# Optimization experiments

Measured on AMD Instinct MI355X. Metric: run time of the kernel, lower is better.

## Reference

```python
import jax, jax.numpy as jnp
import numpy as np

INF = 1e8        # effectively-infinite squared distance (max real value ~3*192^2)
SIGMA = 10.0     # module init arg
CHUNK = 512      # lines processed per block in the min-plus pass
P_FG = 0.005     # sparse foreground probability for the binary mask
N = 192


def _dt1d_last(f):
    """Exact 1D squared-EDT min-plus transform along the last axis.

    d[..., i] = min_j f[..., j] + (i - j)^2, computed brute-force per line,
    chunked over lines to bound memory ([CHUNK, n, n] per block).
    """
    n = f.shape[-1]
    idx = jnp.arange(n, dtype=f.dtype)
    q = (idx[:, None] - idx[None, :]) ** 2              # [n_out, n_in]
    flat = f.reshape(-1, n)
    m = flat.shape[0]
    pad = (-m) % CHUNK
    blocks = jnp.pad(flat, ((0, pad), (0, 0)), constant_values=0.0)
    blocks = blocks.reshape(-1, CHUNK, n)               # [nblk, CHUNK, n]

    def body(b):                                        # b: [CHUNK, n]
        return jnp.min(b[:, None, :] + q[None, :, :], axis=-1)

    out = jax.lax.map(body, blocks).reshape(-1, n)[:m]
    return out.reshape(f.shape)


def _edt(seed, shape_ndim):
    """Euclidean distance to nearest True voxel of `seed` (scipy edt semantics:
    distance_transform_edt(a) == distance to nearest zero of a, i.e. seed = (a == 0))."""
    f = jnp.where(seed, 0.0, INF).astype(jnp.float32)
    for ax in range(shape_ndim):
        f = jnp.moveaxis(_dt1d_last(jnp.moveaxis(f, ax, -1)), -1, ax)
    return jnp.sqrt(f)


def setup_inputs() -> dict:
    key = jax.random.key(0)
    # sparse binary foreground mask (float 0/1), matching a label mask input
    x = (jax.random.uniform(key, (N, N, N)) < P_FG).astype(jnp.float32)
    return {"x": x}


def reference(x) -> jnp.ndarray:
    nd = x.ndim
    d_fg = _edt(x == 0, nd)   # edt(x):      distance to nearest zero of x
    d_bg = _edt(x != 0, nd)   # edt(x == 0): distance to nearest nonzero of x
    return jnp.tanh((d_fg - d_bg) / SIGMA)
```

## Files before the change

kernel.cpp:

```cpp
#include <hip/hip_runtime.h>


typedef unsigned short u16;
typedef unsigned int   u32;
typedef unsigned long long u64;
typedef u16 u16x2 __attribute__((ext_vector_type(2)));

#define NN    192
#define NN2   (192 * 192)
#define NN3   (192 * 192 * 192)

#define PAIRS 8
#define PADL  40
#define SROW  278
#define SENT16 50000
#define SENTPK 0xC350C350u

__device__ __forceinline__ u16x2 pkmin(u16x2 a, u16x2 b) { return __builtin_elementwise_min(a, b); }
__device__ __forceinline__ u16x2 pkmax(u16x2 a, u16x2 b) { return __builtin_elementwise_max(a, b); }
__device__ __forceinline__ u32 pkm32(u32 a, u32 b) {
    return __builtin_bit_cast(u32, pkmin(__builtin_bit_cast(u16x2, a), __builtin_bit_cast(u16x2, b)));
}

__device__ __forceinline__ u64 shr_pair(u64 lo, u64 hi, int s) {
    return (lo >> s) | (s ? (hi << ((64 - s) & 63)) : 0ULL);
}
__device__ __forceinline__ int dist3(u64 a0, u64 a1, u64 a2, int s) {
    u64 w0 = shr_pair(a0, a1, s);
    u64 w1 = shr_pair(a1, a2, s);
    u64 w2 = a2 >> s;
    int t0 = w0 ? __builtin_ctzll(w0) : 255;
    int t1 = w1 ? 64 + __builtin_ctzll(w1) : 255;
    int t2 = w2 ? 128 + __builtin_ctzll(w2) : 255;
    int r = t0 < t1 ? t0 : t1;
    return r < t2 ? r : t2;
}
__device__ __forceinline__ void line_edt(u64 m0, u64 m1, u64 m2, int lane,
                                         u16& o0, u16& o1, u16& o2) {
    u64 r0 = __builtin_bitreverse64(m2);
    u64 r1 = __builtin_bitreverse64(m1);
    u64 r2 = __builtin_bitreverse64(m0);
    const int s = lane, t = 63 - lane;
    int f0 = dist3(m0, m1, m2, s);
    int f1 = dist3(m1, m2, 0ULL, s);
    int f2 = dist3(m2, 0ULL, 0ULL, s);
    int b0 = dist3(r2, 0ULL, 0ULL, t);
    int b1 = dist3(r1, r2, 0ULL, t);
    int b2 = dist3(r0, r1, r2, t);
    int d0 = f0 < b0 ? f0 : b0;
    int d1 = f1 < b1 ? f1 : b1;
    int d2 = f2 < b2 ? f2 : b2;
    o0 = (d0 > 191) ? (u16)65535 : (u16)(d0 * d0);
    o1 = (d1 > 191) ? (u16)65535 : (u16)(d1 * d1);
    o2 = (d2 > 191) ? (u16)65535 : (u16)(d2 * d2);
}

__global__ __launch_bounds__(256) void sdt_scan_k(const float* __restrict__ x,
                                                  u16* __restrict__ A,
                                                  u16* __restrict__ B) {
    const int lane = threadIdx.x & 63;
    const int wid = blockIdx.x * 4 + (threadIdx.x >> 6);
    const size_t base = (size_t)wid * NN;
    float v0 = x[base + lane];
    float v1 = x[base + lane + 64];
    float v2 = x[base + lane + 128];
    u64 m0 = __ballot(v0 != 0.0f);
    u64 m1 = __ballot(v1 != 0.0f);
    u64 m2 = __ballot(v2 != 0.0f);
    u16 a0, a1, a2, b0, b1, b2;
    line_edt(~m0, ~m1, ~m2, lane, a0, a1, a2);
    line_edt(m0, m1, m2, lane, b0, b1, b2);
    A[base + lane] = a0; A[base + lane + 64] = a1; A[base + lane + 128] = a2;
    B[base + lane] = b0; B[base + lane + 64] = b1; B[base + lane + 128] = b2;
}

__device__ __forceinline__ void pad_init(u32* ldsw) {
    for (int idx = threadIdx.x; idx < PAIRS * 86; idx += 512) {
        int p = idx / 86, c = idx - p * 86;
        int word = (c < PADL) ? c : (c + NN);
        ldsw[p * SROW + word] = SENTPK;
    }
}

template<long ES>
__device__ __forceinline__ void stage_in(const u16* __restrict__ f, size_t base, u32* ldsw) {
    for (int idx = threadIdx.x; idx < NN * 2; idx += 512) {
        int j = idx >> 1, q = idx & 1;
        uint4 v = *(const uint4*)(f + base + (size_t)j * ES + 8 * q);
        int a = PADL + j;
        ldsw[(4 * q + 0) * SROW + a] = pkm32(v.x, SENTPK);
        ldsw[(4 * q + 1) * SROW + a] = pkm32(v.y, SENTPK);
        ldsw[(4 * q + 2) * SROW + a] = pkm32(v.z, SENTPK);
        ldsw[(4 * q + 3) * SROW + a] = pkm32(v.w, SENTPK);
    }
}

template<long ES>
__device__ __forceinline__ void stage_out(u16* __restrict__ f, size_t base, const u32* ldsw) {
    for (int idx = threadIdx.x; idx < NN * 2; idx += 512) {
        int j = idx >> 1, q = idx & 1;
        int a = PADL + j;
        uint4 v;
        v.x = ldsw[(4 * q + 0) * SROW + a];
        v.y = ldsw[(4 * q + 1) * SROW + a];
        v.z = ldsw[(4 * q + 2) * SROW + a];
        v.w = ldsw[(4 * q + 3) * SROW + a];
        *(uint4*)(f + base + (size_t)j * ES + 8 * q) = v;
    }
}

__device__ __forceinline__ void full_row(const u16x2* rp, int i0, int i1, int i2,
                                         u16x2& d0, u16x2& d1, u16x2& d2) {
    const float fi0 = (float)i0, fi1 = (float)i1, fi2 = (float)i2;
    float e0l = 3e38f, e0h = 3e38f, e1l = 3e38f, e1h = 3e38f, e2l = 3e38f, e2h = 3e38f;
    for (int j = 0; j < NN; ++j) {
        u16x2 gv = rp[j];
        float gl = (float)gv.x, gh = (float)gv.y;
        float jf = (float)j;
        float t0 = jf - fi0, t1 = jf - fi1, t2 = jf - fi2;
        float s0 = t0 * t0, s1 = t1 * t1, s2 = t2 * t2;
        e0l = fminf(e0l, s0 + gl); e0h = fminf(e0h, s0 + gh);
        e1l = fminf(e1l, s1 + gl); e1h = fminf(e1h, s1 + gh);
        e2l = fminf(e2l, s2 + gl); e2h = fminf(e2h, s2 + gh);
    }
    d0.x = (u16)fminf((float)d0.x, e0l); d0.y = (u16)fminf((float)d0.y, e0h);
    d1.x = (u16)fminf((float)d1.x, e1l); d1.y = (u16)fminf((float)d1.y, e1h);
    d2.x = (u16)fminf((float)d2.x, e2l); d2.y = (u16)fminf((float)d2.y, e2h);
}

__device__ __forceinline__ void expand_tile(u32* ldsw) {
    const int lane = threadIdx.x & 63;
    const int w = threadIdx.x >> 6;
    const int i0 = lane, i1 = lane + 64, i2 = lane + 128;
    u16x2* rp = (u16x2*)(ldsw + w * SROW + PADL);
    u16x2 d0 = rp[i0], d1 = rp[i1], d2 = rp[i2];

    int r = 1;
    bool conv = false;
    while (true) {
#pragma unroll
        for (int m = 0; m < 8; ++m) {
            const int rad = r + m;
            const u16 c = (u16)(rad * rad);
            const u16x2 q = {c, c};
            d0 = pkmin(d0, rp[i0 - rad] + q); d0 = pkmin(d0, rp[i0 + rad] + q);
            d1 = pkmin(d1, rp[i1 - rad] + q); d1 = pkmin(d1, rp[i1 + rad] + q);
            d2 = pkmin(d2, rp[i2 - rad] + q); d2 = pkmin(d2, rp[i2 + rad] + q);
        }
        u16x2 mv = pkmax(pkmax(d0, d1), d2);
        unsigned mm = (mv.x > mv.y) ? mv.x : mv.y;
        unsigned thr = (unsigned)((r + 8) * (r + 8));
        if (__all(mm <= thr)) { conv = true; break; }
        r += 8;
        if (r > 33) break;
    }
    if (!conv) {
        u16x2 mv = pkmax(pkmax(d0, d1), d2);
        unsigned mm = (mv.x > mv.y) ? mv.x : mv.y;
        if (__any(mm > 1681u)) {
            full_row(rp, i0, i1, i2, d0, d1, d2);
        }
    }
    rp[i0] = d0; rp[i1] = d1; rp[i2] = d2;
}

__device__ __forceinline__ int unswizzle(int u) {
    int blk = u >> 4, rem = u & 15;
    int s = rem >> 3, p7 = rem & 7;
    int pid = blk * 8 + p7;
    return 2 * pid + s;
}

__global__ __launch_bounds__(512, 8) void sdt_p2(u16* __restrict__ A, u16* __restrict__ B) {
    __shared__ __align__(16) u32 ldsw[PAIRS * SROW];
    int g = blockIdx.x;
    u16* f = (g < 2304) ? B : A;
    int t = unswizzle((g < 2304) ? g : g - 2304);
    const int gp = t / 12, gk = t - 12 * gp;
    const size_t base = (size_t)gp * NN2 + (size_t)gk * 16;
    pad_init(ldsw);
    stage_in<NN>(f, base, ldsw);
    __syncthreads();
    expand_tile(ldsw);
    __syncthreads();
    stage_out<NN>(f, base, ldsw);
}

__global__ __launch_bounds__(512, 8) void sdt_p3f(u16* __restrict__ B,
                                                  const u16* __restrict__ A,
                                                  float* __restrict__ out) {
    __shared__ __align__(16) u32 ldsw[PAIRS * SROW];
    const int tid = threadIdx.x;
    const int t = unswizzle(blockIdx.x);
    const int gp = t / 12, gk = t - 12 * gp;
    const size_t base = (size_t)gp * NN + (size_t)gk * 16;

    pad_init(ldsw);
    stage_in<NN2>(A, base, ldsw);
    __syncthreads();
    expand_tile(ldsw);
    __syncthreads();
    uint4 va = {0, 0, 0, 0};
    if (tid < NN * 2) {
        int j = tid >> 1, q = tid & 1, a = PADL + j;
        va.x = ldsw[(4 * q + 0) * SROW + a];
        va.y = ldsw[(4 * q + 1) * SROW + a];
        va.z = ldsw[(4 * q + 2) * SROW + a];
        va.w = ldsw[(4 * q + 3) * SROW + a];
    }
    __syncthreads();
    stage_in<NN2>(B, base, ldsw);
    __syncthreads();
    expand_tile(ldsw);
    __syncthreads();
    if (tid < NN * 2) {
        int j = tid >> 1, q = tid & 1, a = PADL + j;
        uint4 vb;
        vb.x = ldsw[(4 * q + 0) * SROW + a];
        vb.y = ldsw[(4 * q + 1) * SROW + a];
        vb.z = ldsw[(4 * q + 2) * SROW + a];
        vb.w = ldsw[(4 * q + 3) * SROW + a];
        u32 wa[4] = {va.x, va.y, va.z, va.w};
        u32 wb[4] = {vb.x, vb.y, vb.z, vb.w};
        float o[8];
#pragma unroll
        for (int s = 0; s < 4; ++s) {
            u16x2 A2 = __builtin_bit_cast(u16x2, wa[s]);
            u16x2 B2 = __builtin_bit_cast(u16x2, wb[s]);
            float x0 = (sqrtf((float)A2.x) - sqrtf((float)B2.x)) * 0.1f;
            float x1 = (sqrtf((float)A2.y) - sqrtf((float)B2.y)) * 0.1f;
            float e0 = __expf(2.f * x0);
            float e1 = __expf(2.f * x1);
            o[2 * s]     = 1.f - 2.f * __builtin_amdgcn_rcpf(e0 + 1.f);
            o[2 * s + 1] = 1.f - 2.f * __builtin_amdgcn_rcpf(e1 + 1.f);
        }
        size_t ga = base + (size_t)j * NN2 + 8 * q;
        *(float4*)(out + ga)     = *(float4*)(o);
        *(float4*)(out + ga + 4) = *(float4*)(o + 4);
    }
}

extern "C" void kernel_launch(void* const* d_in, const int* in_sizes, int n_in,
                              void* d_out, int out_size, void* d_ws, size_t ws_size,
                              hipStream_t stream) {
    const float* x = (const float*)d_in[0];
    u16* A = (u16*)d_ws;
    u16* B = (u16*)((char*)d_ws + (size_t)NN3 * 2);
    float* out = (float*)d_out;

    sdt_scan_k<<<NN2 / 4, 256, 0, stream>>>(x, A, B);
    sdt_p2<<<4608, 512, 0, stream>>>(A, B);
    sdt_p3f<<<2304, 512, 0, stream>>>(B, A, out);
}
```

Measured before the change: 68.91 us.

## Process A and B fields concurrently in 1024-thread blocks for passes two and three

Each block now holds both the A and B tiles in LDS and uses 1024 threads, with 16 waves each expanding one row. In pass three this removes the serial A-then-B phases and their extra barriers. In pass two it halves the block count by pairing the two fields in one block. The cost is double the LDS per block and larger blocks, which may lower occupancy or scheduling flexibility. The `__launch_bounds__(1024, 8)` hint is also likely unattainable.

```diff
diff --git a/kernel.cpp b/kernel.cpp
--- a/kernel.cpp
+++ b/kernel.cpp
@@ -13,6 +13,7 @@
 #define PAIRS 8
 #define PADL  40
 #define SROW  278
+#define HALF  (PAIRS * SROW)
 #define SENT16 50000
 #define SENTPK 0xC350C350u
 
@@ -74,37 +75,41 @@
     B[base + lane] = b0; B[base + lane + 64] = b1; B[base + lane + 128] = b2;
 }
 
-__device__ __forceinline__ void pad_init(u32* ldsw) {
-    for (int idx = threadIdx.x; idx < PAIRS * 86; idx += 512) {
-        int p = idx / 86, c = idx - p * 86;
+__device__ __forceinline__ void pad_init2(u32* ldsw) {
+    for (int idx = threadIdx.x; idx < 2 * PAIRS * 86; idx += 1024) {
+        int h = idx >= PAIRS * 86;
+        int r = idx - h * (PAIRS * 86);
+        int p = r / 86, c = r - p * 86;
         int word = (c < PADL) ? c : (c + NN);
-        ldsw[p * SROW + word] = SENTPK;
+        ldsw[h * HALF + p * SROW + word] = SENTPK;
     }
 }
 
 template<long ES>
-__device__ __forceinline__ void stage_in(const u16* __restrict__ f, size_t base, u32* ldsw) {
-    for (int idx = threadIdx.x; idx < NN * 2; idx += 512) {
+__device__ __forceinline__ void stage_in_h(const u16* __restrict__ f, size_t base,
+                                           u32* dst, int idx) {
+    if (idx < NN * 2) {
         int j = idx >> 1, q = idx & 1;
         uint4 v = *(const uint4*)(f + base + (size_t)j * ES + 8 * q);
         int a = PADL + j;
-        ldsw[(4 * q + 0) * SROW + a] = pkm32(v.x, SENTPK);
-        ldsw[(4 * q + 1) * SROW + a] = pkm32(v.y, SENTPK);
-        ldsw[(4 * q + 2) * SROW + a] = pkm32(v.z, SENTPK);
-        ldsw[(4 * q + 3) * SROW + a] = pkm32(v.w, SENTPK);
+        dst[(4 * q + 0) * SROW + a] = pkm32(v.x, SENTPK);
+        dst[(4 * q + 1) * SROW + a] = pkm32(v.y, SENTPK);
+        dst[(4 * q + 2) * SROW + a] = pkm32(v.z, SENTPK);
+        dst[(4 * q + 3) * SROW + a] = pkm32(v.w, SENTPK);
     }
 }
 
 template<long ES>
-__device__ __forceinline__ void stage_out(u16* __restrict__ f, size_t base, const u32* ldsw) {
-    for (int idx = threadIdx.x; idx < NN * 2; idx += 512) {
+__device__ __forceinline__ void stage_out_h(u16* __restrict__ f, size_t base,
+                                            const u32* src, int idx) {
+    if (idx < NN * 2) {
         int j = idx >> 1, q = idx & 1;
         int a = PADL + j;
         uint4 v;
-        v.x = ldsw[(4 * q + 0) * SROW + a];
-        v.y = ldsw[(4 * q + 1) * SROW + a];
-        v.z = ldsw[(4 * q + 2) * SROW + a];
-        v.w = ldsw[(4 * q + 3) * SROW + a];
+        v.x = src[(4 * q + 0) * SROW + a];
+        v.y = src[(4 * q + 1) * SROW + a];
+        v.z = src[(4 * q + 2) * SROW + a];
+        v.w = src[(4 * q + 3) * SROW + a];
         *(uint4*)(f + base + (size_t)j * ES + 8 * q) = v;
     }
 }
@@ -128,11 +133,10 @@
     d2.x = (u16)fminf((float)d2.x, e2l); d2.y = (u16)fminf((float)d2.y, e2h);
 }
 
-__device__ __forceinline__ void expand_tile(u32* ldsw) {
+__device__ __forceinline__ void expand_row(u32* rowbase) {
     const int lane = threadIdx.x & 63;
-    const int w = threadIdx.x >> 6;
     const int i0 = lane, i1 = lane + 64, i2 = lane + 128;
-    u16x2* rp = (u16x2*)(ldsw + w * SROW + PADL);
+    u16x2* rp = (u16x2*)rowbase;
     u16x2 d0 = rp[i0], d1 = rp[i1], d2 = rp[i2];
 
     int r = 1;
@@ -171,55 +175,57 @@
     return 2 * pid + s;
 }
 
-__global__ __launch_bounds__(512, 8) void sdt_p2(u16* __restrict__ A, u16* __restrict__ B) {
-    __shared__ __align__(16) u32 ldsw[PAIRS * SROW];
-    int g = blockIdx.x;
-    u16* f = (g < 2304) ? B : A;
-    int t = unswizzle((g < 2304) ? g : g - 2304);
+__global__ __launch_bounds__(1024, 8) void sdt_p2(u16* __restrict__ A, u16* __restrict__ B) {
+    __shared__ __align__(16) u32 ldsw[2 * HALF];
+    const int tid = threadIdx.x;
+    const int t = unswizzle(blockIdx.x);
     const int gp = t / 12, gk = t - 12 * gp;
     const size_t base = (size_t)gp * NN2 + (size_t)gk * 16;
-    pad_init(ldsw);
-    stage_in<NN>(f, base, ldsw);
-    __syncthreads();
-    expand_tile(ldsw);
-    __syncthreads();
-    stage_out<NN>(f, base, ldsw);
-}
-
-__global__ __launch_bounds__(512, 8) void sdt_p3f(u16* __restrict__ B,
-                                                  const u16* __restrict__ A,
-                                                  float* __restrict__ out) {
-    __shared__ __align__(16) u32 ldsw[PAIRS * SROW];
+
+    pad_init2(ldsw);
+    if (tid < 512) stage_in_h<NN>(B, base, ldsw, tid);
+    else           stage_in_h<NN>(A, base, ldsw + HALF, tid - 512);
+    __syncthreads();
+    {
+        const int w = tid >> 6;
+        u32* rowbase = ldsw + (w >> 3) * HALF + (w & 7) * SROW + PADL;
+        expand_row(rowbase);
+    }
+    __syncthreads();
+    if (tid < 512) stage_out_h<NN>(B, base, ldsw, tid);
+    else           stage_out_h<NN>(A, base, ldsw + HALF, tid - 512);
+}
+
+__global__ __launch_bounds__(1024, 8) void sdt_p3f(u16* __restrict__ B,
+                                                   const u16* __restrict__ A,
+                                                   float* __restrict__ out) {
+    __shared__ __align__(16) u32 ldsw[2 * HALF];
     const int tid = threadIdx.x;
     const int t = unswizzle(blockIdx.x);
     const int gp = t / 12, gk = t - 12 * gp;
     const size_t base = (size_t)gp * NN + (size_t)gk * 16;
 
-    pad_init(ldsw);
-    stage_in<NN2>(A, base, ldsw);
-    __syncthreads();
-    expand_tile(ldsw);
-    __syncthreads();
-    uint4 va = {0, 0, 0, 0};
+    pad_init2(ldsw);
+    if (tid < 512) stage_in_h<NN2>(A, base, ldsw, tid);
+    else           stage_in_h<NN2>(B, base, ldsw + HALF, tid - 512);
+    __syncthreads();
+    {
+        const int w = tid >> 6;
+        u32* rowbase = ldsw + (w >> 3) * HALF + (w & 7) * SROW + PADL;
+        expand_row(rowbase);
+    }
+    __syncthreads();
     if (tid < NN * 2) {
         int j = tid >> 1, q = tid & 1, a = PADL + j;
+        uint4 va, vb;
         va.x = ldsw[(4 * q + 0) * SROW + a];
         va.y = ldsw[(4 * q + 1) * SROW + a];
         va.z = ldsw[(4 * q + 2) * SROW + a];
         va.w = ldsw[(4 * q + 3) * SROW + a];
-    }
-    __syncthreads();
-    stage_in<NN2>(B, base, ldsw);
-    __syncthreads();
-    expand_tile(ldsw);
-    __syncthreads();
-    if (tid < NN * 2) {
-        int j = tid >> 1, q = tid & 1, a = PADL + j;
-        uint4 vb;
-        vb.x = ldsw[(4 * q + 0) * SROW + a];
-        vb.y = ldsw[(4 * q + 1) * SROW + a];
-        vb.z = ldsw[(4 * q + 2) * SROW + a];
-        vb.w = ldsw[(4 * q + 3) * SROW + a];
+        vb.x = ldsw[HALF + (4 * q + 0) * SROW + a];
+        vb.y = ldsw[HALF + (4 * q + 1) * SROW + a];
+        vb.z = ldsw[HALF + (4 * q + 2) * SROW + a];
+        vb.w = ldsw[HALF + (4 * q + 3) * SROW + a];
         u32 wa[4] = {va.x, va.y, va.z, va.w};
         u32 wb[4] = {vb.x, vb.y, vb.z, vb.w};
         float o[8];
@@ -249,6 +255,6 @@
     float* out = (float*)d_out;
 
     sdt_scan_k<<<NN2 / 4, 256, 0, stream>>>(x, A, B);
-    sdt_p2<<<4608, 512, 0, stream>>>(A, B);
-    sdt_p3f<<<2304, 512, 0, stream>>>(B, A, out);
-}
+    sdt_p2<<<2304, 1024, 0, stream>>>(A, B);
+    sdt_p3f<<<2304, 1024, 0, stream>>>(B, A, out);
+}
```

Result: slower. 74.97 us (+8.8%).
